# Performance work log

Hardware: AMD Instinct MI355X
Metric: run time of the kernel (lower is better)

The kernel has to match this reference:

```python
import jax, jax.numpy as jnp
import numpy as np

D_MODEL = 1024
NUM_HEADS = 16
HEAD_DIM = D_MODEL // NUM_HEADS


def setup_inputs() -> dict:
    key = jax.random.key(0)
    ks = jax.random.split(key, 5)
    scale = 0.02
    return {
        "x": jax.random.normal(ks[0], (1, 4096, D_MODEL), dtype=jnp.float32),
        "w_qkv": jax.random.normal(ks[1], (D_MODEL, 3 * D_MODEL), dtype=jnp.float32) * scale,
        "b_qkv": jax.random.normal(ks[2], (3 * D_MODEL,), dtype=jnp.float32) * scale,
        "w_out": jax.random.normal(ks[3], (D_MODEL, D_MODEL), dtype=jnp.float32) * scale,
        "b_out": jax.random.normal(ks[4], (D_MODEL,), dtype=jnp.float32) * scale,
    }


def reference(x, w_qkv, b_qkv, w_out, b_out):
    B, S, D = x.shape
    H, Hd = NUM_HEADS, HEAD_DIM
    qkv = x @ w_qkv + b_qkv  # [B,S,3D]
    q, k, v = jnp.split(qkv, 3, axis=-1)
    # [B,H,S,Hd]
    q = q.reshape(B, S, H, Hd).transpose(0, 2, 1, 3)
    k = k.reshape(B, S, H, Hd).transpose(0, 2, 1, 3)
    v = v.reshape(B, S, H, Hd).transpose(0, 2, 1, 3)
    scores = jnp.einsum("bhqd,bhkd->bhqk", q, k) / jnp.sqrt(jnp.float32(Hd))
    causal = jnp.tril(jnp.ones((S, S), dtype=bool))
    scores = jnp.where(causal[None, None, :, :], scores, -jnp.inf)
    attn = jax.nn.softmax(scores, axis=-1)  # dropout_p = 0.0 -> identity
    ctx = jnp.einsum("bhqk,bhkd->bhqd", attn, v)
    ctx = ctx.transpose(0, 2, 1, 3).reshape(B, S, D)
    return ctx @ w_out + b_out
```

## Files before the change

### kernel.cpp

```cpp
#include <hip/hip_runtime.h>

#define S 4096
#define DM 1024
#define NH 16
#define HD 64

typedef __attribute__((ext_vector_type(8))) short bf8;
typedef __attribute__((ext_vector_type(4))) float f4;
typedef __attribute__((ext_vector_type(4))) short s4;
typedef __attribute__((ext_vector_type(4))) unsigned int u4;

#define MFMA __builtin_amdgcn_mfma_f32_16x16x32_bf16

#define QSCALE 0.18033688011112042f

static __device__ __forceinline__ unsigned short f2b(float f) {
  unsigned int u = __builtin_bit_cast(unsigned int, f);
  u += 0x7fffu + ((u >> 16) & 1u);
  return (unsigned short)(u >> 16);
}
static __device__ __forceinline__ float b2f(unsigned short u) {
  return __builtin_bit_cast(float, (unsigned int)u << 16);
}

static __device__ __forceinline__ void gld_lds(const unsigned short* g, unsigned short* l) {
  __builtin_amdgcn_global_load_lds(
      (const __attribute__((address_space(1))) unsigned int*)g,
      (__attribute__((address_space(3))) unsigned int*)l, 16, 0, 0);
}

__global__ void prep(const float* __restrict__ x, const float* __restrict__ w_qkv,
                     const float* __restrict__ w_out,
                     unsigned short* __restrict__ xb, unsigned short* __restrict__ wqkvT,
                     unsigned short* __restrict__ woutT) {
  __shared__ float tile[64][65];
  int b = blockIdx.x, t = threadIdx.x;
  if (b < 4096) {
    int i = (b * 256 + t) * 4;
    float4 v = *(const float4*)(x + i);
    s4 o;
    o.x = (short)f2b(v.x); o.y = (short)f2b(v.y);
    o.z = (short)f2b(v.z); o.w = (short)f2b(v.w);
    *(s4*)(xb + i) = o;
    return;
  }
  const float* in; unsigned short* out; int R, C, tc, tr;
  if (b < 4096 + 768) { int bb = b - 4096; in = w_qkv; out = wqkvT; R = DM; C = 3 * DM; tc = bb % 48; tr = bb / 48; }
  else                { int bb = b - 4864; in = w_out; out = woutT; R = DM; C = DM;     tc = bb % 16; tr = bb / 16; }
  int c = t & 63, rbase = (t >> 6) * 16;
#pragma unroll
  for (int i = 0; i < 16; i++) {
    int r = rbase + i;
    tile[r][c] = in[(tr * 64 + r) * C + tc * 64 + c];
  }
  __syncthreads();
#pragma unroll
  for (int i = 0; i < 16; i++) {
    int cc = rbase + i;
    out[(tc * 64 + cc) * R + tr * 64 + c] = f2b(tile[c][cc]);
  }
}


__global__ void __launch_bounds__(256, 2) gemm_qkv(const unsigned short* __restrict__ A,
                                                   const unsigned short* __restrict__ Bt,
                                                   const float* __restrict__ bias,
                                                   unsigned short* __restrict__ Qo,
                                                   unsigned short* __restrict__ Ko,
                                                   unsigned short* __restrict__ Vt) {
  __shared__ unsigned short lA[128 * 32];
  __shared__ unsigned short lB[128 * 32];
  int bid = blockIdx.x;
  int nb = bid % 24, mb = bid / 24;
  int m0 = mb * 128, n0 = nb * 128;
  int t = threadIdx.x, w = t >> 6, lane = t & 63;
  int col = lane & 15, quad = lane >> 4;
  int wm = (w >> 1) * 64, wn = (w & 1) * 64;

  int srow = lane >> 2;
  int sphys = lane & 3;

  f4 acc[4][4];
#pragma unroll
  for (int x = 0; x < 4; x++)
#pragma unroll
    for (int y = 0; y < 4; y++) acc[x][y] = (f4){0.f, 0.f, 0.f, 0.f};

  for (int k0 = 0; k0 < DM; k0 += 32) {
    __syncthreads();
#pragma unroll
    for (int p = 0; p < 2; p++) {
      int j = 2 * w + p;
      int row = j * 16 + srow;
      int lch = sphys ^ ((srow >> 1) & 3);
      gld_lds(A + (size_t)(m0 + row) * DM + k0 + lch * 8, lA + j * 512);
      gld_lds(Bt + (size_t)(n0 + row) * DM + k0 + lch * 8, lB + j * 512);
    }
    __syncthreads();

    bf8 af[4], bfr[4];
#pragma unroll
    for (int x = 0; x < 4; x++) {
      int rA = wm + x * 16 + col;
      af[x] = *(const bf8*)(lA + rA * 32 + (quad ^ ((col >> 1) & 3)) * 8);
      int rB = wn + x * 16 + col;
      bfr[x] = *(const bf8*)(lB + rB * 32 + (quad ^ ((col >> 1) & 3)) * 8);
    }
#pragma unroll
    for (int x = 0; x < 4; x++)
#pragma unroll
      for (int y = 0; y < 4; y++)
        acc[x][y] = MFMA(af[x], bfr[y], acc[x][y], 0, 0, 0);
  }

#pragma unroll
  for (int x = 0; x < 4; x++) {
    int s0r = m0 + wm + x * 16 + quad * 4;
#pragma unroll
    for (int y = 0; y < 4; y++) {
      f4 a = acc[x][y];
      int n = n0 + wn + y * 16 + col;
      float bv = bias[n];
      if (n < 2048) {
        unsigned short* dst = (n < 1024) ? Qo : Ko;
        float sc = (n < 1024) ? QSCALE : 1.0f;
        int nn = n & 1023;
        int hh = nn >> 6, d = nn & 63;
        unsigned short* pp = dst + ((size_t)hh * S + s0r) * HD + d;
#pragma unroll
        for (int r = 0; r < 4; r++) pp[r * HD] = f2b((a[r] + bv) * sc);
      } else {
        int nn = n - 2048;
        int hh = nn >> 6, d = nn & 63;
        s4 pk;
        pk.x = (short)f2b(a[0] + bv);
        pk.y = (short)f2b(a[1] + bv);
        pk.z = (short)f2b(a[2] + bv);
        pk.w = (short)f2b(a[3] + bv);
        *(s4*)(Vt + ((size_t)hh * HD + d) * S + s0r) = pk;
      }
    }
  }
}

__global__ void __launch_bounds__(256, 2) gemm_out(const unsigned short* __restrict__ A,
                                                   const unsigned short* __restrict__ Bt,
                                                   const float* __restrict__ bias,
                                                   float* __restrict__ out) {
  __shared__ unsigned short lA[64 * 32];
  __shared__ unsigned short lB[128 * 32];
  int bid = blockIdx.x;
  int nb = bid % 8, mb = bid / 8;
  int m0 = mb * 64, n0 = nb * 128;
  int t = threadIdx.x, w = t >> 6, lane = t & 63;
  int col = lane & 15, quad = lane >> 4;
  int wm = (w >> 1) * 32, wn = (w & 1) * 64;

  int srow = lane >> 2;
  int sphys = lane & 3;

  f4 acc[2][4];
#pragma unroll
  for (int x = 0; x < 2; x++)
#pragma unroll
    for (int y = 0; y < 4; y++) acc[x][y] = (f4){0.f, 0.f, 0.f, 0.f};

  for (int k0 = 0; k0 < DM; k0 += 32) {
    __syncthreads();
    {
      int j = w;
      int row = j * 16 + srow;
      int lch = sphys ^ ((srow >> 1) & 3);
      gld_lds(A + (size_t)(m0 + row) * DM + k0 + lch * 8, lA + j * 512);
    }
#pragma unroll
    for (int p = 0; p < 2; p++) {
      int j = 2 * w + p;
      int row = j * 16 + srow;
      int lch = sphys ^ ((srow >> 1) & 3);
      gld_lds(Bt + (size_t)(n0 + row) * DM + k0 + lch * 8, lB + j * 512);
    }
    __syncthreads();

    bf8 af[2], bfr[4];
#pragma unroll
    for (int x = 0; x < 2; x++) {
      int rA = wm + x * 16 + col;
      af[x] = *(const bf8*)(lA + rA * 32 + (quad ^ ((col >> 1) & 3)) * 8);
    }
#pragma unroll
    for (int y = 0; y < 4; y++) {
      int rB = wn + y * 16 + col;
      bfr[y] = *(const bf8*)(lB + rB * 32 + (quad ^ ((col >> 1) & 3)) * 8);
    }
#pragma unroll
    for (int x = 0; x < 2; x++)
#pragma unroll
      for (int y = 0; y < 4; y++)
        acc[x][y] = MFMA(af[x], bfr[y], acc[x][y], 0, 0, 0);
  }

#pragma unroll
  for (int x = 0; x < 2; x++) {
    int s0r = m0 + wm + x * 16 + quad * 4;
#pragma unroll
    for (int y = 0; y < 4; y++) {
      f4 a = acc[x][y];
      int n = n0 + wn + y * 16 + col;
      float bv = bias[n];
#pragma unroll
      for (int r = 0; r < 4; r++) out[(size_t)(s0r + r) * DM + n] = a[r] + bv;
    }
  }
}

__global__ void __launch_bounds__(128, 4) attn(const unsigned short* __restrict__ Q,
                                               const unsigned short* __restrict__ K,
                                               const unsigned short* __restrict__ Vt,
                                               unsigned short* __restrict__ slabA,
                                               unsigned short* __restrict__ slab1,
                                               unsigned short* __restrict__ slab2,
                                               unsigned short* __restrict__ slab3,
                                               float* __restrict__ l0_g,
                                               float* __restrict__ l1_g,
                                               float* __restrict__ l2_g,
                                               float* __restrict__ l3_g) {
  __shared__ unsigned short kbuf[64 * 64];
  __shared__ unsigned short vbuf[64 * 64];

  int bid = blockIdx.x;
  int h = bid / 160;
  int j = 159 - (bid % 160);
  int qb, c0, nst, p;
  if (j < 16) {
    qb = j; c0 = 0; nst = qb + 1; p = 0;
  } else if (j < 64) {
    int u = j - 16;
    qb = 16 + (u >> 1);
    int half = u & 1;
    int ntot = qb + 1, nh = (ntot + 1) >> 1;
    p = half;
    if (half) { c0 = nh; nst = ntot - nh; }
    else      { c0 = 0;  nst = nh; }
  } else {
    int u = j - 64;
    qb = 40 + (u >> 2);
    int qt = u & 3;
    int ntot = qb + 1;
    int base = ntot >> 2, rem = ntot & 3;
    c0 = qt * base + (qt < rem ? qt : rem);
    nst = base + (qt < rem ? 1 : 0);
    p = qt;
  }
  bool single = (qb < 16);
  int q0blk = qb * 64;
  int t = threadIdx.x, w = t >> 6, lane = t & 63;
  int col = lane & 15, quad = lane >> 4;
  int q0 = q0blk + w * 32;

  const unsigned short* Qh = Q + (size_t)h * S * HD;
  const unsigned short* Kh = K + (size_t)h * S * HD;
  const unsigned short* Vh = Vt + (size_t)h * HD * S;

  bf8 qf[2][2];
#pragma unroll
  for (int g = 0; g < 2; g++) {
    qf[g][0] = *(const bf8*)(Qh + (q0 + g * 16 + col) * HD + quad * 8);
    qf[g][1] = *(const bf8*)(Qh + (q0 + g * 16 + col) * HD + 32 + quad * 8);
  }

  f4 o[2][4];
#pragma unroll
  for (int g = 0; g < 2; g++)
#pragma unroll
    for (int dt = 0; dt < 4; dt++) o[g][dt] = (f4){0.f, 0.f, 0.f, 0.f};
  float lsum[2] = {0.f, 0.f};

  int srow = lane >> 3;
  int sphys = lane & 7;

  for (int s_ = 0; s_ < nst; s_++) {
    int kv0 = (c0 + s_) * 64;
    __syncthreads();
#pragma unroll
    for (int pp = 0; pp < 4; pp++) {
      int jj = 4 * w + pp;
      int row = jj * 8 + srow;
      int lch = sphys ^ (row & 7);
      gld_lds(Kh + (size_t)(kv0 + row) * HD + lch * 8, kbuf + jj * 512);
      gld_lds(Vh + (size_t)row * S + kv0 + lch * 8, vbuf + jj * 512);
    }
    __syncthreads();

    f4 st[2][4];
#pragma unroll
    for (int tt = 0; tt < 4; tt++) {
      int kr = tt * 16 + col;
      int sw = col & 7;
      bf8 ka = *(const bf8*)(kbuf + kr * 64 + (quad ^ sw) * 8);
      bf8 kb = *(const bf8*)(kbuf + kr * 64 + ((quad + 4) ^ sw) * 8);
#pragma unroll
      for (int g = 0; g < 2; g++) {
        f4 z = {0.f, 0.f, 0.f, 0.f};
        z = MFMA(ka, qf[g][0], z, 0, 0, 0);
        z = MFMA(kb, qf[g][1], z, 0, 0, 0);
        st[g][tt] = z;
      }
    }

#pragma unroll
    for (int g = 0; g < 2; g++) {
      int q16 = q0 + g * 16;
      if (kv0 + 63 > q16) {
        int q = q16 + col;
#pragma unroll
        for (int tt = 0; tt < 4; tt++)
#pragma unroll
          for (int rr = 0; rr < 4; rr++) {
            int kv = kv0 + tt * 16 + quad * 4 + rr;
            st[g][tt][rr] = (kv <= q) ? st[g][tt][rr] : -1e30f;
          }
      }
    }

    bf8 pf[2][2];
#pragma unroll
    for (int g = 0; g < 2; g++) {
      float pv[4][4];
#pragma unroll
      for (int tt = 0; tt < 4; tt++) {
#pragma unroll
        for (int rr = 0; rr < 4; rr++) pv[tt][rr] = __builtin_amdgcn_exp2f(st[g][tt][rr]);
        lsum[g] += (pv[tt][0] + pv[tt][1]) + (pv[tt][2] + pv[tt][3]);
      }
#pragma unroll
      for (int f = 0; f < 2; f++) {
        unsigned int a0, a1, b0, b1;
        asm("v_cvt_pk_bf16_f32 %0, %1, %2" : "=v"(a0) : "v"(pv[2 * f][0]),     "v"(pv[2 * f][1]));
        asm("v_cvt_pk_bf16_f32 %0, %1, %2" : "=v"(a1) : "v"(pv[2 * f][2]),     "v"(pv[2 * f][3]));
        asm("v_cvt_pk_bf16_f32 %0, %1, %2" : "=v"(b0) : "v"(pv[2 * f + 1][0]), "v"(pv[2 * f + 1][1]));
        asm("v_cvt_pk_bf16_f32 %0, %1, %2" : "=v"(b1) : "v"(pv[2 * f + 1][2]), "v"(pv[2 * f + 1][3]));
        asm("v_permlane32_swap_b32 %0, %1" : "+v"(a0), "+v"(b0));
        asm("v_permlane32_swap_b32 %0, %1" : "+v"(a1), "+v"(b1));
        asm("v_permlane16_swap_b32 %0, %1" : "+v"(a0), "+v"(b0));
        asm("v_permlane16_swap_b32 %0, %1" : "+v"(a1), "+v"(b1));
        u4 pk;
        pk.x = a0; pk.y = a1; pk.z = b0; pk.w = b1;
        pf[g][f] = __builtin_bit_cast(bf8, pk);
      }
    }

#pragma unroll
    for (int dt = 0; dt < 4; dt++) {
      int vr = dt * 16 + col;
      int sw = col & 7;
      bf8 v0 = *(const bf8*)(vbuf + vr * 64 + (quad ^ sw) * 8);
      bf8 v1 = *(const bf8*)(vbuf + vr * 64 + ((quad + 4) ^ sw) * 8);
#pragma unroll
      for (int g = 0; g < 2; g++) {
        o[g][dt] = MFMA(pf[g][0], v0, o[g][dt], 0, 0, 0);
        o[g][dt] = MFMA(pf[g][1], v1, o[g][dt], 0, 0, 0);
      }
    }
  }

#pragma unroll
  for (int g = 0; g < 2; g++) {
    float ls = lsum[g];
    ls += __shfl_xor(ls, 16);
    ls += __shfl_xor(ls, 32);
    int q16 = q0 + g * 16;
    if (single) {
      float inv = 1.0f / ls;
      float ir[4];
#pragma unroll
      for (int rr = 0; rr < 4; rr++) ir[rr] = __shfl(inv, quad * 4 + rr);
#pragma unroll
      for (int dt = 0; dt < 4; dt++)
#pragma unroll
        for (int rr = 0; rr < 4; rr++) {
          int row = q16 + quad * 4 + rr;
          slabA[(size_t)row * DM + h * HD + dt * 16 + col] = f2b(o[g][dt][rr] * ir[rr]);
        }
    } else {
      unsigned short* slab; int rowbase; float* lg;
      if (p == 0)      { slab = slabA; rowbase = q16;        lg = l0_g; }
      else if (p == 1) { slab = slab1; rowbase = q16 - 1024; lg = l1_g; }
      else if (p == 2) { slab = slab2; rowbase = q16 - 2560; lg = l2_g; }
      else             { slab = slab3; rowbase = q16 - 2560; lg = l3_g; }
      if (quad == 0) lg[h * S + q16 + col] = ls;
#pragma unroll
      for (int dt = 0; dt < 4; dt++)
#pragma unroll
        for (int rr = 0; rr < 4; rr++) {
          int row = rowbase + quad * 4 + rr;
          slab[(size_t)row * DM + h * HD + dt * 16 + col] = f2b(o[g][dt][rr]);
        }
    }
  }
}

__global__ void combine(unsigned short* __restrict__ Ctx,
                        const unsigned short* __restrict__ slab1,
                        const unsigned short* __restrict__ slab2,
                        const unsigned short* __restrict__ slab3,
                        const float* __restrict__ l0_g,
                        const float* __restrict__ l1_g,
                        const float* __restrict__ l2_g,
                        const float* __restrict__ l3_g) {
  int row = 1024 + blockIdx.x;
  int cc = threadIdx.x * 4;
  int h = cc >> 6;
  s4 a = *(const s4*)(Ctx + (size_t)row * DM + cc);
  s4 b = *(const s4*)(slab1 + (size_t)(row - 1024) * DM + cc);
  float acc0 = b2f((unsigned short)a.x) + b2f((unsigned short)b.x);
  float acc1 = b2f((unsigned short)a.y) + b2f((unsigned short)b.y);
  float acc2 = b2f((unsigned short)a.z) + b2f((unsigned short)b.z);
  float acc3 = b2f((unsigned short)a.w) + b2f((unsigned short)b.w);
  float l = l0_g[h * S + row] + l1_g[h * S + row];
  if (row >= 2560) {
    s4 c = *(const s4*)(slab2 + (size_t)(row - 2560) * DM + cc);
    s4 d = *(const s4*)(slab3 + (size_t)(row - 2560) * DM + cc);
    acc0 += b2f((unsigned short)c.x) + b2f((unsigned short)d.x);
    acc1 += b2f((unsigned short)c.y) + b2f((unsigned short)d.y);
    acc2 += b2f((unsigned short)c.z) + b2f((unsigned short)d.z);
    acc3 += b2f((unsigned short)c.w) + b2f((unsigned short)d.w);
    l += l2_g[h * S + row] + l3_g[h * S + row];
  }
  float inv = 1.0f / l;
  s4 o;
  o.x = (short)f2b(acc0 * inv);
  o.y = (short)f2b(acc1 * inv);
  o.z = (short)f2b(acc2 * inv);
  o.w = (short)f2b(acc3 * inv);
  *(s4*)(Ctx + (size_t)row * DM + cc) = o;
}

extern "C" void kernel_launch(void* const* d_in, const int* in_sizes, int n_in,
                              void* d_out, int out_size, void* d_ws, size_t ws_size,
                              hipStream_t stream) {
  const float* x     = (const float*)d_in[0];
  const float* w_qkv = (const float*)d_in[1];
  const float* b_qkv = (const float*)d_in[2];
  const float* w_out = (const float*)d_in[3];
  const float* b_out = (const float*)d_in[4];
  float* out = (float*)d_out;

  char* ws = (char*)d_ws;
  unsigned short* xb    = (unsigned short*)(ws);
  unsigned short* wqkvT = (unsigned short*)(ws + (size_t)8  * 1048576);
  unsigned short* woutT = (unsigned short*)(ws + (size_t)14 * 1048576);
  unsigned short* Qb    = (unsigned short*)(ws + (size_t)16 * 1048576);
  unsigned short* Kb    = (unsigned short*)(ws + (size_t)24 * 1048576);
  unsigned short* Vtb   = (unsigned short*)(ws + (size_t)32 * 1048576);
  unsigned short* ctx   = (unsigned short*)(ws + (size_t)40 * 1048576);

  unsigned short* slab1 = xb;
  float* l0_g = (float*)(ws + (size_t)6 * 1048576);
  float* l1_g = (float*)(ws + (size_t)6 * 1048576 + 256 * 1024);
  float* l2_g = (float*)(ws + (size_t)6 * 1048576 + 512 * 1024);
  float* l3_g = (float*)(ws + (size_t)6 * 1048576 + 768 * 1024);
  unsigned short* slab2 = wqkvT;
  unsigned short* slab3 = (unsigned short*)(ws + (size_t)11 * 1048576);

  prep<<<5120, 256, 0, stream>>>(x, w_qkv, w_out, xb, wqkvT, woutT);
  gemm_qkv<<<32 * 24, 256, 0, stream>>>(xb, wqkvT, b_qkv, Qb, Kb, Vtb);
  attn<<<NH * 160, 128, 0, stream>>>(Qb, Kb, Vtb, ctx, slab1, slab2, slab3,
                                     l0_g, l1_g, l2_g, l3_g);
  combine<<<3072, 256, 0, stream>>>(ctx, slab1, slab2, slab3, l0_g, l1_g, l2_g, l3_g);
  gemm_out<<<64 * 8, 256, 0, stream>>>(ctx, woutT, b_out, out);
}
```

Before: 207.5 us.

## Register-prefetch next K tile in QKV GEMM and attention loops

Replaces the direct global-to-LDS loads in the QKV GEMM and the attention K/V loop with global loads into registers, issued one iteration ahead and then stored to LDS. The global latency of the next tile can then overlap the MFMA work on the current tile instead of stalling on a barrier. In exchange it uses more VGPRs, which may lower occupancy, and adds explicit LDS stores plus hand-written waitcnt and barrier sequencing. The output projection GEMM keeps the global_load_lds path.

```diff
diff --git a/kernel.cpp b/kernel.cpp
--- a/kernel.cpp
+++ b/kernel.cpp
@@ -21,12 +21,6 @@
 }
 static __device__ __forceinline__ float b2f(unsigned short u) {
   return __builtin_bit_cast(float, (unsigned int)u << 16);
-}
-
-static __device__ __forceinline__ void gld_lds(const unsigned short* g, unsigned short* l) {
-  __builtin_amdgcn_global_load_lds(
-      (const __attribute__((address_space(1))) unsigned int*)g,
-      (__attribute__((address_space(3))) unsigned int*)l, 16, 0, 0);
 }
 
 __global__ void prep(const float* __restrict__ x, const float* __restrict__ w_qkv,
@@ -86,17 +80,32 @@
 #pragma unroll
     for (int y = 0; y < 4; y++) acc[x][y] = (f4){0.f, 0.f, 0.f, 0.f};
 
-  for (int k0 = 0; k0 < DM; k0 += 32) {
-    __syncthreads();
+  bf8 arg[2], brg[2];
+  auto qload = [&](int k0) {
 #pragma unroll
     for (int p = 0; p < 2; p++) {
       int j = 2 * w + p;
       int row = j * 16 + srow;
       int lch = sphys ^ ((srow >> 1) & 3);
-      gld_lds(A + (size_t)(m0 + row) * DM + k0 + lch * 8, lA + j * 512);
-      gld_lds(Bt + (size_t)(n0 + row) * DM + k0 + lch * 8, lB + j * 512);
-    }
-    __syncthreads();
+      arg[p] = *(const bf8*)(A + (size_t)(m0 + row) * DM + k0 + lch * 8);
+      brg[p] = *(const bf8*)(Bt + (size_t)(n0 + row) * DM + k0 + lch * 8);
+    }
+  };
+  qload(0);
+
+  for (int k0 = 0; k0 < DM; k0 += 32) {
+    asm volatile("s_waitcnt lgkmcnt(0)" ::: "memory");
+    __builtin_amdgcn_s_barrier();
+#pragma unroll
+    for (int p = 0; p < 2; p++) {
+      int j = 2 * w + p;
+      *(bf8*)(lA + j * 512 + lane * 8) = arg[p];
+      *(bf8*)(lB + j * 512 + lane * 8) = brg[p];
+    }
+    if (k0 + 32 < DM) qload(k0 + 32);
+    asm volatile("s_waitcnt lgkmcnt(0)" ::: "memory");
+    __builtin_amdgcn_s_barrier();
+    __builtin_amdgcn_sched_barrier(0);
 
     bf8 af[4], bfr[4];
 #pragma unroll
@@ -164,6 +173,12 @@
   for (int x = 0; x < 2; x++)
 #pragma unroll
     for (int y = 0; y < 4; y++) acc[x][y] = (f4){0.f, 0.f, 0.f, 0.f};
+
+  auto gld_lds = [](const unsigned short* g, unsigned short* l) {
+    __builtin_amdgcn_global_load_lds(
+        (const __attribute__((address_space(1))) unsigned int*)g,
+        (__attribute__((address_space(3))) unsigned int*)l, 16, 0, 0);
+  };
 
   for (int k0 = 0; k0 < DM; k0 += 32) {
     __syncthreads();
@@ -279,18 +294,37 @@
   int srow = lane >> 3;
   int sphys = lane & 7;
 
-  for (int s_ = 0; s_ < nst; s_++) {
-    int kv0 = (c0 + s_) * 64;
-    __syncthreads();
+  bf8 krg[4], vrg[4];
+  auto aload = [&](int s) {
+    int kv0s = (c0 + s) * 64;
 #pragma unroll
     for (int pp = 0; pp < 4; pp++) {
       int jj = 4 * w + pp;
       int row = jj * 8 + srow;
       int lch = sphys ^ (row & 7);
-      gld_lds(Kh + (size_t)(kv0 + row) * HD + lch * 8, kbuf + jj * 512);
-      gld_lds(Vh + (size_t)row * S + kv0 + lch * 8, vbuf + jj * 512);
-    }
-    __syncthreads();
+      krg[pp] = *(const bf8*)(Kh + (size_t)(kv0s + row) * HD + lch * 8);
+      vrg[pp] = *(const bf8*)(Vh + (size_t)row * S + kv0s + lch * 8);
+    }
+  };
+  aload(0);
+
+  for (int s_ = 0; s_ < nst; s_++) {
+    int kv0 = (c0 + s_) * 64;
+
+    asm volatile("s_waitcnt lgkmcnt(0)" ::: "memory");
+    __builtin_amdgcn_s_barrier();
+
+#pragma unroll
+    for (int pp = 0; pp < 4; pp++) {
+      int jj = 4 * w + pp;
+      *(bf8*)(kbuf + jj * 512 + lane * 8) = krg[pp];
+      *(bf8*)(vbuf + jj * 512 + lane * 8) = vrg[pp];
+    }
+    if (s_ + 1 < nst) aload(s_ + 1);
+
+    asm volatile("s_waitcnt lgkmcnt(0)" ::: "memory");
+    __builtin_amdgcn_s_barrier();
+    __builtin_amdgcn_sched_barrier(0);
 
     f4 st[2][4];
 #pragma unroll
```

New measurement: 337.2 us. 1.63x slower.
